# Kernel optimization log

Measured on AMD Instinct MI355X. Metric: run time of the kernel, lower is better.

## Reference

```python
import jax, jax.numpy as jnp
import numpy as np

N, IN_F, OUT_F, K = 256, 1024, 128, 32

def setup_inputs() -> dict:
    key = jax.random.key(0)
    k1, k2 = jax.random.split(key)
    x = jax.random.normal(k1, (N, IN_F), dtype=jnp.float32)
    T = jax.random.normal(k2, (IN_F, OUT_F, K), dtype=jnp.float32)
    return {"x": x, "T": T}

def reference(x, T):
    # matrices: [N, OUT_F, K]
    M = jnp.einsum('ni,iok->nok', x, T)
    # pairwise L1 distance over kernel dim: [N, N, OUT_F]
    norm = jnp.abs(M[:, None, :, :] - M[None, :, :, :]).sum(axis=3)
    expnorm = jnp.exp(-norm)
    # sum over the other-sample axis; subtract self-term exp(0)=1
    o_b = expnorm.sum(axis=0) - 1.0  # [N, OUT_F]
    return jnp.concatenate([x, o_b], axis=1)
```

## Files before the change

### kernel.cpp

```cpp
#include <hip/hip_runtime.h>

typedef unsigned short u16;
typedef __attribute__((ext_vector_type(8))) short short8_t;
typedef __attribute__((ext_vector_type(4))) float f32x4;

#define N_SAMP 256
#define IN_F   1024
#define OUT_F  128
#define KDIM   32
#define JTOT   (OUT_F * KDIM)
#define OUT_ROW (IN_F + OUT_F)

#define CHUNKS 8
#define MPC    32
#define MPW    8

__device__ __forceinline__ u16 f2bf(float f) {
    union { float f; unsigned u; } v; v.f = f;
    unsigned r = v.u + 0x7FFFu + ((v.u >> 16) & 1u);
    return (u16)(r >> 16);
}


__global__ __launch_bounds__(256) void copy_init_conv(const float* __restrict__ x,
                                                      float* __restrict__ out,
                                                      u16* __restrict__ At) {
    int n = blockIdx.x, t = threadIdx.x;
    float4 v = reinterpret_cast<const float4*>(x + (size_t)n * IN_F)[t];
    reinterpret_cast<float4*>(out + (size_t)n * OUT_ROW)[t] = v;
    ushort4 b;
    b.x = f2bf(v.x); b.y = f2bf(v.y); b.z = f2bf(v.z); b.w = f2bf(v.w);
    reinterpret_cast<ushort4*>(At + (size_t)n * IN_F)[t] = b;
}

__global__ __launch_bounds__(256) void convT_kernel(const float* __restrict__ T,
                                                    u16* __restrict__ Bt) {
    __shared__ float Ls[64 * 65];
    const int t = threadIdx.x;
    const int j0 = blockIdx.x * 64, k0 = blockIdx.y * 64;
    const int r = t >> 2, c4 = t & 3;

    const float4* src = reinterpret_cast<const float4*>(T + (size_t)(k0 + r) * JTOT + j0 + c4 * 16);
    float4 v0 = src[0], v1 = src[1], v2 = src[2], v3 = src[3];
    float vv[16] = {v0.x,v0.y,v0.z,v0.w, v1.x,v1.y,v1.z,v1.w,
                    v2.x,v2.y,v2.z,v2.w, v3.x,v3.y,v3.z,v3.w};
#pragma unroll
    for (int i = 0; i < 16; ++i) Ls[r * 65 + c4 * 16 + i] = vv[i];
    __syncthreads();

    unsigned pk[8];
#pragma unroll
    for (int i = 0; i < 8; ++i) {
        u16 lo = f2bf(Ls[(c4 * 16 + 2 * i    ) * 65 + r]);
        u16 hi = f2bf(Ls[(c4 * 16 + 2 * i + 1) * 65 + r]);
        pk[i] = (unsigned)lo | ((unsigned)hi << 16);
    }
    uint4* dst = reinterpret_cast<uint4*>(Bt + (size_t)(j0 + r) * IN_F + k0 + c4 * 16);
    dst[0] = make_uint4(pk[0], pk[1], pk[2], pk[3]);
    dst[1] = make_uint4(pk[4], pk[5], pk[6], pk[7]);
}

#define LDB 136
__global__ __launch_bounds__(128) void mfma_gemm(const u16* __restrict__ At,
                                                 const u16* __restrict__ Bt,
                                                 float* __restrict__ Mt) {
    __shared__ u16 Bs[64 * LDB];
    __shared__ u16 As[32 * LDB];
    const int t = threadIdx.x;
    const int w = t >> 6, l = t & 63;
    const int jb = blockIdx.x * 64, nb = blockIdx.y * 32;
    const int rb = t >> 1, hb = t & 1;
    const int ra = t >> 2, qa = t & 3;

    f32x4 acc00 = {0.f,0.f,0.f,0.f}, acc01 = {0.f,0.f,0.f,0.f};
    f32x4 acc10 = {0.f,0.f,0.f,0.f}, acc11 = {0.f,0.f,0.f,0.f};

    float4 sb[8], sa[4];
    auto LOADG = [&](int it) {
        const float4* gb = reinterpret_cast<const float4*>(Bt + (size_t)(jb + rb) * IN_F + it * 128 + hb * 64);
#pragma unroll
        for (int i = 0; i < 8; ++i) sb[i] = gb[i];
        const float4* ga = reinterpret_cast<const float4*>(At + (size_t)(nb + ra) * IN_F + it * 128 + qa * 32);
#pragma unroll
        for (int i = 0; i < 4; ++i) sa[i] = ga[i];
    };
    auto STORE = [&]() {
#pragma unroll
        for (int i = 0; i < 8; ++i) *reinterpret_cast<float4*>(&Bs[rb * LDB + hb * 64 + i * 8]) = sb[i];
#pragma unroll
        for (int i = 0; i < 4; ++i) *reinterpret_cast<float4*>(&As[ra * LDB + qa * 32 + i * 8]) = sa[i];
    };

    LOADG(0); STORE(); __syncthreads();

    for (int it = 0; it < 8; ++it) {
        if (it < 7) LOADG(it + 1);
#pragma unroll
        for (int s = 0; s < 4; ++s) {
            const int co = s * 32 + 8 * (l >> 4);
            short8_t a0 = *reinterpret_cast<const short8_t*>(&Bs[(w * 32 +      (l & 15)) * LDB + co]);
            short8_t a1 = *reinterpret_cast<const short8_t*>(&Bs[(w * 32 + 16 + (l & 15)) * LDB + co]);
            short8_t b0 = *reinterpret_cast<const short8_t*>(&As[(          (l & 15)) * LDB + co]);
            short8_t b1 = *reinterpret_cast<const short8_t*>(&As[(     16 + (l & 15)) * LDB + co]);
            acc00 = __builtin_amdgcn_mfma_f32_16x16x32_bf16(a0, b0, acc00, 0, 0, 0);
            acc01 = __builtin_amdgcn_mfma_f32_16x16x32_bf16(a0, b1, acc01, 0, 0, 0);
            acc10 = __builtin_amdgcn_mfma_f32_16x16x32_bf16(a1, b0, acc10, 0, 0, 0);
            acc11 = __builtin_amdgcn_mfma_f32_16x16x32_bf16(a1, b1, acc11, 0, 0, 0);
        }
        __syncthreads();
        if (it < 7) { STORE(); __syncthreads(); }
    }

    const int jrow = jb + w * 32 + (l >> 4) * 4;
    const int ncol = nb + (l & 15);
#pragma unroll
    for (int r = 0; r < 4; ++r) {
        Mt[(size_t)(jrow + r     ) * N_SAMP + ncol     ] = acc00[r];
        Mt[(size_t)(jrow + r     ) * N_SAMP + ncol + 16] = acc01[r];
        Mt[(size_t)(jrow + 16 + r) * N_SAMP + ncol     ] = acc10[r];
        Mt[(size_t)(jrow + 16 + r) * N_SAMP + ncol + 16] = acc11[r];
    }
}

__global__ __launch_bounds__(256) void dist_part(const float* __restrict__ Mt,
                                                 float* __restrict__ part) {
    __shared__ float Mo[MPC][36];
    __shared__ float Pred[4][N_SAMP];
    const int t = threadIdx.x, w = t >> 6, l = t & 63;
    const int o  = blockIdx.x;
    const int mb = blockIdx.y * MPC;

    {
        const int m = t & 31, kb = (t >> 5) * 4;
#pragma unroll
        for (int kk = 0; kk < 4; ++kk)
            Mo[m][kb + kk] = Mt[(size_t)(o * KDIM + kb + kk) * N_SAMP + mb + m];
    }
    __syncthreads();

    float accd[4][MPW];
#pragma unroll
    for (int r = 0; r < 4; ++r)
#pragma unroll
        for (int m = 0; m < MPW; ++m) accd[r][m] = 0.f;

#pragma unroll
    for (int kh = 0; kh < 4; ++kh) {
        float r0[8], r1[8], r2[8], r3[8];
#pragma unroll
        for (int k = 0; k < 8; ++k) {
            const float* p = Mt + (size_t)(o * KDIM + kh * 8 + k) * N_SAMP + l;
            r0[k] = p[0]; r1[k] = p[64]; r2[k] = p[128]; r3[k] = p[192];
        }
#pragma unroll
        for (int m = 0; m < MPW; ++m) {
            float mo[8];
#pragma unroll
            for (int i = 0; i < 2; ++i)
                *reinterpret_cast<float4*>(&mo[i * 4]) =
                    *reinterpret_cast<const float4*>(&Mo[w * MPW + m][kh * 8 + i * 4]);
#pragma unroll
            for (int k = 0; k < 8; ++k) {
                accd[0][m] += fabsf(r0[k] - mo[k]);
                accd[1][m] += fabsf(r1[k] - mo[k]);
                accd[2][m] += fabsf(r2[k] - mo[k]);
                accd[3][m] += fabsf(r3[k] - mo[k]);
            }
        }
    }

    float a0 = 0.f, a1 = 0.f, a2 = 0.f, a3 = 0.f;
#pragma unroll
    for (int m = 0; m < MPW; ++m) {
        a0 += __expf(-accd[0][m]); a1 += __expf(-accd[1][m]);
        a2 += __expf(-accd[2][m]); a3 += __expf(-accd[3][m]);
    }
    Pred[w][l] = a0; Pred[w][l + 64] = a1; Pred[w][l + 128] = a2; Pred[w][l + 192] = a3;
    __syncthreads();

    {
        float s = Pred[0][t] + Pred[1][t] + Pred[2][t] + Pred[3][t];
        part[(size_t)blockIdx.y * (OUT_F * N_SAMP) + o * N_SAMP + t] = s;
    }
}

__global__ __launch_bounds__(128) void dist_reduce(const float* __restrict__ part,
                                                   float* __restrict__ out) {
    const int n = blockIdx.x, t = threadIdx.x;
    float s = -1.0f;
#pragma unroll
    for (int c = 0; c < CHUNKS; ++c)
        s += part[(size_t)c * (OUT_F * N_SAMP) + t * N_SAMP + n];
    out[(size_t)n * OUT_ROW + IN_F + t] = s;
}

__global__ __launch_bounds__(256) void copy_init_kernel(const float* __restrict__ x,
                                                        float* __restrict__ out) {
    int n = blockIdx.x, t = threadIdx.x;
    reinterpret_cast<float4*>(out + (size_t)n * OUT_ROW)[t] =
        reinterpret_cast<const float4*>(x + (size_t)n * IN_F)[t];
    if (t < OUT_F) out[(size_t)n * OUT_ROW + IN_F + t] = -1.0f;
}

#define BM 64
#define BN 64
#define BK 16
#define AS_STRIDE 68
__global__ __launch_bounds__(256) void gemm_kernel(const float* __restrict__ x,
                                                   const float* __restrict__ T,
                                                   float* __restrict__ M) {
    __shared__ float As_[BK][AS_STRIDE];
    __shared__ float Bs_[BK][BN];
    const int jb = blockIdx.x * BN, nb = blockIdx.y * BM;
    const int t = threadIdx.x, tx = t & 15, ty = t >> 4;
    float acc[4][4] = {};
    for (int k0 = 0; k0 < IN_F; k0 += BK) {
        {
            int row = t >> 2, cg = (t & 3) * 4;
            float4 v = *reinterpret_cast<const float4*>(&x[(size_t)(nb + row) * IN_F + k0 + cg]);
            As_[cg + 0][row] = v.x; As_[cg + 1][row] = v.y;
            As_[cg + 2][row] = v.z; As_[cg + 3][row] = v.w;
        }
        {
            int r = t >> 4, cg = (t & 15) * 4;
            *reinterpret_cast<float4*>(&Bs_[r][cg]) =
                *reinterpret_cast<const float4*>(&T[(size_t)(k0 + r) * JTOT + jb + cg]);
        }
        __syncthreads();
#pragma unroll
        for (int kk = 0; kk < BK; ++kk) {
            float4 av = *reinterpret_cast<const float4*>(&As_[kk][ty * 4]);
            float4 bv = *reinterpret_cast<const float4*>(&Bs_[kk][tx * 4]);
            float a[4] = {av.x, av.y, av.z, av.w}, b[4] = {bv.x, bv.y, bv.z, bv.w};
#pragma unroll
            for (int i = 0; i < 4; ++i)
#pragma unroll
                for (int j = 0; j < 4; ++j) acc[i][j] += a[i] * b[j];
        }
        __syncthreads();
    }
#pragma unroll
    for (int i = 0; i < 4; ++i) {
        int n = nb + ty * 4 + i;
        float4 v = make_float4(acc[i][0], acc[i][1], acc[i][2], acc[i][3]);
        *reinterpret_cast<float4*>(&M[(size_t)n * JTOT + jb + tx * 4]) = v;
    }
}

__global__ __launch_bounds__(256) void dist_kernel(const float* __restrict__ M,
                                                   float* __restrict__ out) {
    __shared__ float Mo_[64][KDIM];
    const int o = blockIdx.x >> 2, chunk = blockIdx.x & 3, t = threadIdx.x;
    float r[KDIM];
    const float4* mrow = reinterpret_cast<const float4*>(&M[(size_t)t * JTOT + o * KDIM]);
#pragma unroll
    for (int f = 0; f < 8; ++f) {
        float4 v = mrow[f];
        r[f*4+0]=v.x; r[f*4+1]=v.y; r[f*4+2]=v.z; r[f*4+3]=v.w;
    }
    const int mbase = chunk * 64;
    {
        int row = t >> 3, f4 = t & 7;
        *reinterpret_cast<float4*>(&Mo_[row][f4*4]) =
            *reinterpret_cast<const float4*>(&M[(size_t)(mbase+row)*JTOT + o*KDIM + f4*4]);
        *reinterpret_cast<float4*>(&Mo_[row+32][f4*4]) =
            *reinterpret_cast<const float4*>(&M[(size_t)(mbase+row+32)*JTOT + o*KDIM + f4*4]);
    }
    __syncthreads();
    float acc = 0.f;
    for (int m = 0; m < 64; ++m) {
        float d = 0.f;
#pragma unroll
        for (int k = 0; k < KDIM; ++k) d += fabsf(r[k] - Mo_[m][k]);
        acc += __expf(-d);
    }
    atomicAdd(&out[(size_t)t * OUT_ROW + IN_F + o], acc);
}

extern "C" void kernel_launch(void* const* d_in, const int* in_sizes, int n_in,
                              void* d_out, int out_size, void* d_ws, size_t ws_size,
                              hipStream_t stream) {
    const float* x = (const float*)d_in[0];
    const float* T = (const float*)d_in[1];
    float* out = (float*)d_out;

    const size_t MT_BYTES = (size_t)JTOT * N_SAMP * 4;
    const size_t AT_BYTES = (size_t)N_SAMP * IN_F * 2;
    const size_t BT_BYTES = (size_t)JTOT * IN_F * 2;

    if (ws_size >= MT_BYTES + AT_BYTES + BT_BYTES) {
        float* Mt = (float*)d_ws;
        u16*   At = (u16*)((char*)d_ws + MT_BYTES);
        u16*   Bt = (u16*)((char*)d_ws + MT_BYTES + AT_BYTES);
        float* part = (float*)Bt;

        copy_init_conv<<<N_SAMP, 256, 0, stream>>>(x, out, At);
        convT_kernel<<<dim3(JTOT / 64, IN_F / 64), 256, 0, stream>>>(T, Bt);
        mfma_gemm<<<dim3(JTOT / 64, N_SAMP / 32), 128, 0, stream>>>(At, Bt, Mt);
        dist_part<<<dim3(OUT_F, CHUNKS), 256, 0, stream>>>(Mt, part);
        dist_reduce<<<N_SAMP, 128, 0, stream>>>(part, out);
    } else {
        float* M = (float*)d_ws;
        copy_init_kernel<<<N_SAMP, 256, 0, stream>>>(x, out);
        dim3 ggrid(JTOT / BN, N_SAMP / BM);
        gemm_kernel<<<ggrid, 256, 0, stream>>>(x, T, M);
        dist_kernel<<<OUT_F * 4, 256, 0, stream>>>(M, out);
    }
}
```

Baseline: 120.5 us.

## Fuse prep kernels, double-buffer GEMM shared memory, transpose reduce indexing

Merges the x copy/bf16 conversion into the T transpose-conversion kernel, which removes one launch. Double-buffers the A/B shared-memory tiles in the MFMA GEMM so each iteration needs one barrier instead of two. Reorganizes dist_reduce so threads index along the contiguous sample axis for coalesced reads of the partial sums; the strided writes move to the output instead. Double buffering doubles the GEMM's LDS footprint, which may reduce occupancy.

```diff
diff --git a/kernel.cpp b/kernel.cpp
--- a/kernel.cpp
+++ b/kernel.cpp
@@ -22,19 +22,11 @@
 }
 
 
-__global__ __launch_bounds__(256) void copy_init_conv(const float* __restrict__ x,
-                                                      float* __restrict__ out,
-                                                      u16* __restrict__ At) {
-    int n = blockIdx.x, t = threadIdx.x;
-    float4 v = reinterpret_cast<const float4*>(x + (size_t)n * IN_F)[t];
-    reinterpret_cast<float4*>(out + (size_t)n * OUT_ROW)[t] = v;
-    ushort4 b;
-    b.x = f2bf(v.x); b.y = f2bf(v.y); b.z = f2bf(v.z); b.w = f2bf(v.w);
-    reinterpret_cast<ushort4*>(At + (size_t)n * IN_F)[t] = b;
-}
-
-__global__ __launch_bounds__(256) void convT_kernel(const float* __restrict__ T,
-                                                    u16* __restrict__ Bt) {
+__global__ __launch_bounds__(256) void prep_kernel(const float* __restrict__ x,
+                                                   const float* __restrict__ T,
+                                                   float* __restrict__ out,
+                                                   u16* __restrict__ At,
+                                                   u16* __restrict__ Bt) {
     __shared__ float Ls[64 * 65];
     const int t = threadIdx.x;
     const int j0 = blockIdx.x * 64, k0 = blockIdx.y * 64;
@@ -58,14 +50,23 @@
     uint4* dst = reinterpret_cast<uint4*>(Bt + (size_t)(j0 + r) * IN_F + k0 + c4 * 16);
     dst[0] = make_uint4(pk[0], pk[1], pk[2], pk[3]);
     dst[1] = make_uint4(pk[4], pk[5], pk[6], pk[7]);
+
+    const int bid = blockIdx.y * 64 + blockIdx.x;
+    if (bid < N_SAMP) {
+        float4 v = reinterpret_cast<const float4*>(x + (size_t)bid * IN_F)[t];
+        reinterpret_cast<float4*>(out + (size_t)bid * OUT_ROW)[t] = v;
+        ushort4 b;
+        b.x = f2bf(v.x); b.y = f2bf(v.y); b.z = f2bf(v.z); b.w = f2bf(v.w);
+        reinterpret_cast<ushort4*>(At + (size_t)bid * IN_F)[t] = b;
+    }
 }
 
 #define LDB 136
 __global__ __launch_bounds__(128) void mfma_gemm(const u16* __restrict__ At,
                                                  const u16* __restrict__ Bt,
                                                  float* __restrict__ Mt) {
-    __shared__ u16 Bs[64 * LDB];
-    __shared__ u16 As[32 * LDB];
+    __shared__ u16 Bs[2][64 * LDB];
+    __shared__ u16 As[2][32 * LDB];
     const int t = threadIdx.x;
     const int w = t >> 6, l = t & 63;
     const int jb = blockIdx.x * 64, nb = blockIdx.y * 32;
@@ -84,31 +85,33 @@
 #pragma unroll
         for (int i = 0; i < 4; ++i) sa[i] = ga[i];
     };
-    auto STORE = [&]() {
-#pragma unroll
-        for (int i = 0; i < 8; ++i) *reinterpret_cast<float4*>(&Bs[rb * LDB + hb * 64 + i * 8]) = sb[i];
-#pragma unroll
-        for (int i = 0; i < 4; ++i) *reinterpret_cast<float4*>(&As[ra * LDB + qa * 32 + i * 8]) = sa[i];
+    auto STORE = [&](int b) {
+#pragma unroll
+        for (int i = 0; i < 8; ++i) *reinterpret_cast<float4*>(&Bs[b][rb * LDB + hb * 64 + i * 8]) = sb[i];
+#pragma unroll
+        for (int i = 0; i < 4; ++i) *reinterpret_cast<float4*>(&As[b][ra * LDB + qa * 32 + i * 8]) = sa[i];
     };
 
-    LOADG(0); STORE(); __syncthreads();
-
+    LOADG(0); STORE(0); __syncthreads();
+
+#pragma unroll 2
     for (int it = 0; it < 8; ++it) {
+        const int cur = it & 1;
         if (it < 7) LOADG(it + 1);
 #pragma unroll
         for (int s = 0; s < 4; ++s) {
             const int co = s * 32 + 8 * (l >> 4);
-            short8_t a0 = *reinterpret_cast<const short8_t*>(&Bs[(w * 32 +      (l & 15)) * LDB + co]);
-            short8_t a1 = *reinterpret_cast<const short8_t*>(&Bs[(w * 32 + 16 + (l & 15)) * LDB + co]);
-            short8_t b0 = *reinterpret_cast<const short8_t*>(&As[(          (l & 15)) * LDB + co]);
-            short8_t b1 = *reinterpret_cast<const short8_t*>(&As[(     16 + (l & 15)) * LDB + co]);
+            short8_t a0 = *reinterpret_cast<const short8_t*>(&Bs[cur][(w * 32 +      (l & 15)) * LDB + co]);
+            short8_t a1 = *reinterpret_cast<const short8_t*>(&Bs[cur][(w * 32 + 16 + (l & 15)) * LDB + co]);
+            short8_t b0 = *reinterpret_cast<const short8_t*>(&As[cur][(          (l & 15)) * LDB + co]);
+            short8_t b1 = *reinterpret_cast<const short8_t*>(&As[cur][(     16 + (l & 15)) * LDB + co]);
             acc00 = __builtin_amdgcn_mfma_f32_16x16x32_bf16(a0, b0, acc00, 0, 0, 0);
             acc01 = __builtin_amdgcn_mfma_f32_16x16x32_bf16(a0, b1, acc01, 0, 0, 0);
             acc10 = __builtin_amdgcn_mfma_f32_16x16x32_bf16(a1, b0, acc10, 0, 0, 0);
             acc11 = __builtin_amdgcn_mfma_f32_16x16x32_bf16(a1, b1, acc11, 0, 0, 0);
         }
+        if (it < 7) STORE((it + 1) & 1);
         __syncthreads();
-        if (it < 7) { STORE(); __syncthreads(); }
     }
 
     const int jrow = jb + w * 32 + (l >> 4) * 4;
@@ -184,14 +187,14 @@
     }
 }
 
-__global__ __launch_bounds__(128) void dist_reduce(const float* __restrict__ part,
+__global__ __launch_bounds__(256) void dist_reduce(const float* __restrict__ part,
                                                    float* __restrict__ out) {
-    const int n = blockIdx.x, t = threadIdx.x;
+    const int o = blockIdx.x, n = threadIdx.x;
     float s = -1.0f;
 #pragma unroll
     for (int c = 0; c < CHUNKS; ++c)
-        s += part[(size_t)c * (OUT_F * N_SAMP) + t * N_SAMP + n];
-    out[(size_t)n * OUT_ROW + IN_F + t] = s;
+        s += part[(size_t)c * (OUT_F * N_SAMP) + o * N_SAMP + n];
+    out[(size_t)n * OUT_ROW + IN_F + o] = s;
 }
 
 __global__ __launch_bounds__(256) void copy_init_kernel(const float* __restrict__ x,
@@ -294,11 +297,10 @@
         u16*   Bt = (u16*)((char*)d_ws + MT_BYTES + AT_BYTES);
         float* part = (float*)Bt;
 
-        copy_init_conv<<<N_SAMP, 256, 0, stream>>>(x, out, At);
-        convT_kernel<<<dim3(JTOT / 64, IN_F / 64), 256, 0, stream>>>(T, Bt);
+        prep_kernel<<<dim3(JTOT / 64, IN_F / 64), 256, 0, stream>>>(x, T, out, At, Bt);
         mfma_gemm<<<dim3(JTOT / 64, N_SAMP / 32), 128, 0, stream>>>(At, Bt, Mt);
         dist_part<<<dim3(OUT_F, CHUNKS), 256, 0, stream>>>(Mt, part);
-        dist_reduce<<<N_SAMP, 128, 0, stream>>>(part, out);
+        dist_reduce<<<OUT_F, 256, 0, stream>>>(part, out);
     } else {
         float* M = (float*)d_ws;
         copy_init_kernel<<<N_SAMP, 256, 0, stream>>>(x, out);
```

Measured after the change: 117.8 us. 1.02x faster.
